# Kernel optimization log

Measured on AMD Instinct MI355X. Metric: run time of the kernel, lower is better.

## Reference

```python
import jax, jax.numpy as jnp
import numpy as np


def _pool_matrix(out_size, in_size):
    # torch AdaptiveAvgPool2d bin edges: start=floor(i*in/out), end=ceil((i+1)*in/out)
    starts = (np.arange(out_size) * in_size) // out_size
    ends = -((-(np.arange(1, out_size + 1) * in_size)) // out_size)
    M = np.zeros((out_size, in_size), np.float32)
    for i in range(out_size):
        M[i, starts[i]:ends[i]] = 1.0 / (ends[i] - starts[i])
    return jnp.asarray(M)


def _cbr(x, w, g, b):
    # 1x1 conv (no bias) + BatchNorm eval (rm=0, rv=1, eps=1e-5) + ReLU6
    y = jnp.einsum('bchw,oc->bohw', x, w)
    y = y * (g / np.sqrt(1.0 + 1e-5))[None, :, None, None] + b[None, :, None, None]
    return jnp.clip(y, 0.0, 6.0)


def _fd_gate(x, g, b, scale):
    # x: [..., L, D]; parameter-free finite-difference gate with residual 0.2
    xp = jnp.pad(x, [(0, 0)] * (x.ndim - 2) + [(1, 0), (0, 0)])[..., :-1, :]
    d = x - xp
    mu = d.mean(-1, keepdims=True)
    var = ((d - mu) ** 2).mean(-1, keepdims=True)
    dn = (d - mu) / jnp.sqrt(var + 1e-5) * g + b
    nd = jnp.sqrt((dn ** 2).sum(-1, keepdims=True)) * scale
    gate = 0.2 + 0.8 * jnp.tanh(jnp.abs(nd))
    return x * gate


def _cross_scan(x):  # [B,C,H,W] -> [B,8,C,H*W]
    B, C, H, W = x.shape
    h = jnp.arange(H)[:, None]
    w = jnp.arange(W)[None, :]
    diag = jnp.broadcast_to(((h + w) % W)[None, None], x.shape)
    anti = jnp.broadcast_to(((w - h) % W)[None, None], x.shape)
    x0 = x.reshape(B, C, H * W)
    x1 = x.transpose(0, 1, 3, 2).reshape(B, C, H * W)
    gd = jnp.take_along_axis(x, diag, -1).transpose(0, 1, 3, 2).reshape(B, C, H * W)
    ga = jnp.take_along_axis(x, anti, -1).transpose(0, 1, 3, 2).reshape(B, C, H * W)
    return jnp.stack([x0, x1, jnp.flip(x0, -1), jnp.flip(x1, -1), gd, ga,
                      jnp.flip(gd, -1), jnp.flip(ga, -1)], 1)


def _cross_merge(ys, gw):  # ys [B,8,D,H,W], gw [B,8] -> [B,D,H*W]
    B, K, D, H, W = ys.shape
    L = H * W
    ys = ys.reshape(B, K, D, L) * gw[:, :, None, None]
    h = jnp.arange(H)[:, None]
    w = jnp.arange(W)[None, :]
    y_h = ys[:, 0] + jnp.flip(ys[:, 2], -1)
    y_v = ys[:, 1] + jnp.flip(ys[:, 3], -1)
    y_v = y_v.reshape(B, D, W, H).transpose(0, 1, 3, 2).reshape(B, D, L)
    y_rb = (y_h + y_v).reshape(B, D, H, W)
    y_d = (ys[:, 4] + jnp.flip(ys[:, 6], -1)).reshape(B, D, W, H).transpose(0, 1, 3, 2)
    y_a = (ys[:, 5] + jnp.flip(ys[:, 7], -1)).reshape(B, D, W, H).transpose(0, 1, 3, 2)
    # scatter along W is the inverse permutation of the diagonal gather
    inv_d = jnp.broadcast_to(((w - h) % W)[None, None], y_d.shape)
    inv_a = jnp.broadcast_to(((w + h) % W)[None, None], y_a.shape)
    s_d = jnp.take_along_axis(y_d, inv_d, -1)
    s_a = jnp.take_along_axis(y_a, inv_a, -1)
    return (y_rb + s_d + s_a).reshape(B, D, L)


def _mamba(params, x):  # x [B,L,Dm] -> [B,L,Dm]
    in_w, cw, cb, xp_w, dtp_w, dtp_b, A_log, Dp, out_w = params
    B, L, Dm = x.shape
    d_inner, d_conv = cw.shape
    d_state = A_log.shape[1]
    dt_rank = dtp_w.shape[1]
    xz = x @ in_w.T                       # [B,L,2*d_inner]
    u, z = jnp.split(xz, 2, axis=-1)
    uc = u.transpose(0, 2, 1)             # [B,d_inner,L]
    up = jnp.pad(uc, ((0, 0), (0, 0), (d_conv - 1, 0)))  # causal depthwise conv
    conv = cb[None, :, None]
    for k in range(d_conv):
        conv = conv + cw[None, :, k, None] * up[:, :, k:k + L]
    u = jax.nn.silu(conv).transpose(0, 2, 1)  # [B,L,d_inner]
    x_dbl = u @ xp_w.T
    dt, Bc, Cc = jnp.split(x_dbl, [dt_rank, dt_rank + d_state], axis=-1)
    dt = jax.nn.softplus(dt @ dtp_w.T + dtp_b)  # [B,L,d_inner]
    A = -jnp.exp(A_log)                         # [d_inner,d_state]

    def step(h, inp):
        dt_t, B_t, C_t, u_t = inp               # [B,d_inner],[B,d_state],[B,d_state],[B,d_inner]
        dA = jnp.exp(dt_t[..., None] * A)
        h = dA * h + (dt_t * u_t)[..., None] * B_t[:, None, :]
        y = jnp.einsum('bds,bs->bd', h, C_t)
        return h, y

    h0 = jnp.zeros((B, d_inner, d_state), x.dtype)
    _, ys = jax.lax.scan(step, h0, (dt.swapaxes(0, 1), Bc.swapaxes(0, 1),
                                    Cc.swapaxes(0, 1), u.swapaxes(0, 1)))
    y = ys.swapaxes(0, 1) + u * Dp
    y = y * jax.nn.silu(z)
    return y @ out_w.T


def setup_inputs() -> dict:
    ks = jax.random.split(jax.random.key(0), 12)
    B, C, H, W = 8, 512, 16, 16
    dim, pool_len = 128, 4
    chs = dim * pool_len + C          # 1024
    d_inner, d_state, d_conv, dt_rank = 2048, 16, 4, 64
    f32 = jnp.float32
    inp = {
        'x': jax.random.normal(ks[0], (B, C, H, W), f32),
        'pw': jax.random.normal(ks[1], (pool_len, dim, C), f32) * 0.05,
        'bn_g': jnp.ones((pool_len, dim), f32),
        'bn_b': jnp.zeros((pool_len, dim), f32),
        'gate_w': jax.random.normal(ks[2], (8, chs), f32) * 0.02,
        'ln_g': jnp.ones((chs,), f32),
        'ln_b': jnp.zeros((chs,), f32),
        'fd_scale': jnp.ones((1,), f32),
        'in_w': jax.random.normal(ks[3], (8, 2 * d_inner, chs), f32) * 0.02,
        'cw': jax.random.normal(ks[4], (8, d_inner, d_conv), f32) * 0.2,
        'cb': jnp.zeros((8, d_inner), f32),
        'xp_w': jax.random.normal(ks[5], (8, dt_rank + 2 * d_state, d_inner), f32) * 0.02,
        'dtp_w': jax.random.normal(ks[6], (8, d_inner, dt_rank), f32) * 0.05,
        'dtp_b': jnp.log(jnp.expm1(jax.random.uniform(ks[7], (8, d_inner), f32, 1e-3, 0.1))),
        'A_log': jnp.broadcast_to(jnp.log(jnp.arange(1, d_state + 1, dtype=f32)), (8, d_inner, d_state)) + 0.0,
        'D_p': jnp.ones((8, d_inner), f32),
        'out_w': jax.random.normal(ks[8], (8, chs, d_inner), f32) * 0.02,
    }
    return inp


def reference(x, pw, bn_g, bn_b, gate_w, ln_g, ln_b, fd_scale,
              in_w, cw, cb, xp_w, dtp_w, dtp_b, A_log, D_p, out_w):
    B, C, H, W = x.shape
    dim = pw.shape[1]
    pools = []
    # pool branch 0: ConvBNReLU then global avg pool then bilinear upsample (constant)
    p0 = _cbr(x, pw[0], bn_g[0], bn_b[0]).mean((2, 3), keepdims=True)
    pools.append(jnp.broadcast_to(p0, (B, dim, H, W)))
    for i, s in enumerate((5, 9, 13)):
        M = _pool_matrix(s, H)
        pooled = jnp.einsum('oh,bchw,pw->bcop', M, x, M)
        y = _cbr(pooled, pw[i + 1], bn_g[i + 1], bn_b[i + 1])
        pools.append(jax.image.resize(y, (B, dim, H, W), 'bilinear'))
    pools.append(x)
    xc = jnp.concatenate(pools, 1)                 # [B, chs, H, W]
    chs = xc.shape[1]
    # MoE gating: softmax over 8 directions, keep top-4
    logits = xc.mean((2, 3)) @ gate_w.T
    scores = jax.nn.softmax(logits, -1)
    vals, idx = jax.lax.top_k(scores, 4)
    gw = jnp.zeros_like(scores).at[jnp.arange(B)[:, None], idx].set(vals)
    xs = _cross_scan(xc).transpose(0, 1, 3, 2)     # [B,8,L,chs]
    xg = _fd_gate(xs, ln_g, ln_b, fd_scale)
    params = (in_w, cw, cb, xp_w, dtp_w, dtp_b, A_log, D_p, out_w)
    ys = jax.vmap(_mamba, in_axes=(0, 1), out_axes=1)(params, xg)  # [B,8,L,chs]
    ys = ys.transpose(0, 1, 3, 2).reshape(B, 8, chs, H, W)
    y = _cross_merge(ys, gw)                       # [B,chs,L]
    return y.reshape(B, chs, H, W)
```

## Files before the change

### kernel.cpp

```cpp
#include <hip/hip_runtime.h>
#include <math.h>

#define DEV __device__ __forceinline__

typedef unsigned short u16;
typedef short bf16x8 __attribute__((ext_vector_type(8)));
typedef float f32x4 __attribute__((ext_vector_type(4)));

DEV float blk_sum(float v, float* sb) {
  #pragma unroll
  for (int o = 32; o > 0; o >>= 1) v += __shfl_down(v, o, 64);
  int lane = threadIdx.x & 63, wid = threadIdx.x >> 6;
  __syncthreads();
  if (lane == 0) sb[wid] = v;
  __syncthreads();
  return sb[0] + sb[1] + sb[2] + sb[3];
}

DEV float silu_f(float x) { return x / (1.f + expf(-x)); }
DEV int imin_i(int a, int b) { return a < b ? a : b; }
DEV int imax_i(int a, int b) { return a > b ? a : b; }

DEV u16 bf_rne(float x) {
  unsigned u = __float_as_uint(x);
  return (u16)((u + 0x7fffu + ((u >> 16) & 1u)) >> 16);
}
DEV float bf_val(u16 h) { return __uint_as_float((unsigned)h << 16); }

DEV void gll16(const void* g, void* l) {
  __builtin_amdgcn_global_load_lds(
      (__attribute__((address_space(1))) void*)(g),
      (__attribute__((address_space(3))) void*)(l), 16, 0, 0);
}

#define BN_SCALE 0.9999950000374997f


__global__ __launch_bounds__(256) void copyx_kernel(const float* __restrict__ x,
                                                    float* __restrict__ xcT) {
  int idx = blockIdx.x * 256 + threadIdx.x;
  int l = idx & 255; int bc = idx >> 8; int c = bc & 511; int b = bc >> 9;
  xcT[((long)b * 256 + l) * 1024 + 512 + c] = x[idx];
}

__global__ __launch_bounds__(256) void pool0_kernel(const float* __restrict__ x,
    const float* __restrict__ pw, const float* __restrict__ bng,
    const float* __restrict__ bnb, float* __restrict__ xcT) {
  __shared__ float sb[8];
  int b = blockIdx.x, o = blockIdx.y, p = threadIdx.x;
  const float* xp = x + (long)b * 512 * 256 + p;
  const float* w = pw + (long)o * 512;
  float s = 0.f;
  for (int c = 0; c < 512; c++) s = fmaf(xp[(long)c * 256], w[c], s);
  float gs = bng[o] * BN_SCALE;
  float v = fminf(fmaxf(fmaf(s, gs, bnb[o]), 0.f), 6.f);
  float m = blk_sum(v, sb) * (1.f / 256.f);
  xcT[((long)b * 256 + p) * 1024 + o] = m;
}

__global__ void apool_kernel(const float* __restrict__ x, float* __restrict__ pooled, int s) {
  int s2 = s * s;
  int idx = blockIdx.x * 256 + threadIdx.x;
  if (idx >= 8 * 512 * s2) return;
  int op = idx % s2; int bc = idx / s2;
  int oh = op / s, ow = op % s;
  int h0 = oh * 16 / s, h1 = (oh * 16 + 16 + s - 1) / s;
  int w0 = ow * 16 / s, w1 = (ow * 16 + 16 + s - 1) / s;
  const float* xp = x + (long)bc * 256;
  float sum = 0.f;
  for (int h = h0; h < h1; h++)
    for (int w = w0; w < w1; w++) sum += xp[h * 16 + w];
  pooled[(long)bc * s2 + op] = sum / (float)((h1 - h0) * (w1 - w0));
}

__global__ void cbr_kernel(const float* __restrict__ pooled, const float* __restrict__ pw_i,
    const float* __restrict__ bng_i, const float* __restrict__ bnb_i,
    float* __restrict__ ys, int s2) {
  int b = blockIdx.x, o = blockIdx.y, p = threadIdx.x;
  if (p >= s2) return;
  const float* pp = pooled + (long)b * 512 * s2 + p;
  const float* w = pw_i + (long)o * 512;
  float sum = 0.f;
  for (int c = 0; c < 512; c++) sum = fmaf(pp[(long)c * s2], w[c], sum);
  float gs = bng_i[o] * BN_SCALE;
  ys[((long)b * 128 + o) * s2 + p] = fminf(fmaxf(fmaf(sum, gs, bnb_i[o]), 0.f), 6.f);
}

__global__ void resize_kernel(const float* __restrict__ ys, float* __restrict__ xcT,
                              int s, int ch0) {
  int b = blockIdx.x, o = blockIdx.y, t = threadIdx.x;
  int h = t >> 4, w = t & 15;
  float scale = (float)s / 16.f;
  float sh = (h + 0.5f) * scale - 0.5f;
  float sw = (w + 0.5f) * scale - 0.5f;
  int h0 = (int)floorf(sh); float fh = sh - (float)h0;
  int w0 = (int)floorf(sw); float fw = sw - (float)w0;
  int ha = imin_i(imax_i(h0, 0), s - 1), hb = imin_i(imax_i(h0 + 1, 0), s - 1);
  int wa = imin_i(imax_i(w0, 0), s - 1), wb = imin_i(imax_i(w0 + 1, 0), s - 1);
  const float* yp = ys + ((long)b * 128 + o) * s * s;
  float v = (1.f - fh) * ((1.f - fw) * yp[ha * s + wa] + fw * yp[ha * s + wb]) +
            fh * ((1.f - fw) * yp[hb * s + wa] + fw * yp[hb * s + wb]);
  xcT[((long)b * 256 + t) * 1024 + ch0 + o] = v;
}

__global__ __launch_bounds__(256) void xcmean_kernel(const float* __restrict__ xcT,
                                                     float* __restrict__ xm) {
  int idx = blockIdx.x * 256 + threadIdx.x;
  int c = idx & 1023; int b = idx >> 10;
  const float* p = xcT + (long)b * 256 * 1024 + c;
  float s = 0.f;
  for (int l = 0; l < 256; l++) s += p[(long)l * 1024];
  xm[idx] = s * (1.f / 256.f);
}

__global__ void gate_kernel(const float* __restrict__ xm, const float* __restrict__ gww,
                            float* __restrict__ gwout) {
  __shared__ float lg[64];
  int t = threadIdx.x;
  int b = t >> 3, j = t & 7;
  const float* xb = xm + b * 1024;
  const float* wj = gww + j * 1024;
  float s = 0.f;
  for (int c = 0; c < 1024; c++) s = fmaf(xb[c], wj[c], s);
  lg[t] = s;
  __syncthreads();
  if (t < 8) {
    float v[8], mx = -1e30f;
    for (int i = 0; i < 8; i++) { v[i] = lg[t * 8 + i]; mx = fmaxf(mx, v[i]); }
    float den = 0.f;
    for (int i = 0; i < 8; i++) { v[i] = expf(v[i] - mx); den += v[i]; }
    float inv = 1.f / den;
    float out[8], tmp[8];
    for (int i = 0; i < 8; i++) { out[i] = 0.f; tmp[i] = v[i] * inv; }
    for (int it = 0; it < 4; it++) {
      int bi = 0; float bv = tmp[0];
      for (int i = 1; i < 8; i++) if (tmp[i] > bv) { bv = tmp[i]; bi = i; }
      out[bi] = bv; tmp[bi] = -1e30f;
    }
    for (int i = 0; i < 8; i++) gwout[t * 8 + i] = out[i];
  }
}


DEV int scan_src(int k, int l) {
  switch (k) {
    case 0: return l;
    case 1: return ((l & 15) << 4) | (l >> 4);
    case 2: return 255 - l;
    case 3: { int l2 = 255 - l; return ((l2 & 15) << 4) | (l2 >> 4); }
    case 4: { int h = l & 15, w = l >> 4; return (h << 4) | ((h + w) & 15); }
    case 5: { int h = l & 15, w = l >> 4; return (h << 4) | ((w - h) & 15); }
    case 6: { int l2 = 255 - l; int h = l2 & 15, w = l2 >> 4; return (h << 4) | ((h + w) & 15); }
    default:{ int l2 = 255 - l; int h = l2 & 15, w = l2 >> 4; return (h << 4) | ((w - h) & 15); }
  }
}

__global__ __launch_bounds__(256) void fd_gate_kernel(const float* __restrict__ xcT,
    const float* __restrict__ lng, const float* __restrict__ lnb,
    const float* __restrict__ fsc, u16* __restrict__ xghi, u16* __restrict__ xglo,
    int k0, const float* __restrict__ gw) {
  __shared__ float sb[8];
  int l = blockIdx.x;
  int rg = blockIdx.y;
  int kk = rg >> 3, b = rg & 7;
  int k = k0 + kk;
  if (gw[b * 8 + k] == 0.f) return;
  int t = threadIdx.x;
  int p = scan_src(k, l);
  float4 cv = *((const float4*)(xcT + ((long)b * 256 + p) * 1024) + t);
  float4 pv = make_float4(0.f, 0.f, 0.f, 0.f);
  if (l > 0) {
    int pm = scan_src(k, l - 1);
    pv = *((const float4*)(xcT + ((long)b * 256 + pm) * 1024) + t);
  }
  float d0 = cv.x - pv.x, d1 = cv.y - pv.y, d2 = cv.z - pv.z, d3 = cv.w - pv.w;
  float mu = blk_sum(d0 + d1 + d2 + d3, sb) * (1.f / 1024.f);
  float e0 = d0 - mu, e1 = d1 - mu, e2 = d2 - mu, e3 = d3 - mu;
  float var = blk_sum(e0*e0 + e1*e1 + e2*e2 + e3*e3, sb) * (1.f / 1024.f);
  float rstd = rsqrtf(var + 1e-5f);
  float4 g4 = *((const float4*)lng + t);
  float4 b4 = *((const float4*)lnb + t);
  float n0 = fmaf(e0 * rstd, g4.x, b4.x);
  float n1 = fmaf(e1 * rstd, g4.y, b4.y);
  float n2 = fmaf(e2 * rstd, g4.z, b4.z);
  float n3 = fmaf(e3 * rstd, g4.w, b4.w);
  float ss = blk_sum(n0*n0 + n1*n1 + n2*n2 + n3*n3, sb);
  float nd = sqrtf(ss) * fsc[0];
  float gate = 0.2f + 0.8f * tanhf(fabsf(nd));
  float o0 = cv.x * gate, o1 = cv.y * gate, o2 = cv.z * gate, o3 = cv.w * gate;
  ushort4 h4, l4;
  h4.x = bf_rne(o0); l4.x = bf_rne(o0 - bf_val(h4.x));
  h4.y = bf_rne(o1); l4.y = bf_rne(o1 - bf_val(h4.y));
  h4.z = bf_rne(o2); l4.z = bf_rne(o2 - bf_val(h4.z));
  h4.w = bf_rne(o3); l4.w = bf_rne(o3 - bf_val(h4.w));
  long off = ((long)rg * 256 + l) * 1024;
  ((ushort4*)(xghi + off))[t] = h4;
  ((ushort4*)(xglo + off))[t] = l4;
}

__global__ __launch_bounds__(256) void split_kernel(const float* __restrict__ src,
    u16* __restrict__ hi, u16* __restrict__ lo, long n4) {
  long i = (long)blockIdx.x * 256 + threadIdx.x;
  if (i >= n4) return;
  float4 v = ((const float4*)src)[i];
  ushort4 h, l;
  h.x = bf_rne(v.x); l.x = bf_rne(v.x - bf_val(h.x));
  h.y = bf_rne(v.y); l.y = bf_rne(v.y - bf_val(h.y));
  h.z = bf_rne(v.z); l.z = bf_rne(v.z - bf_val(h.z));
  h.w = bf_rne(v.w); l.w = bf_rne(v.w - bf_val(h.w));
  ((ushort4*)hi)[i] = h;
  ((ushort4*)lo)[i] = l;
}

template<int EPI>
__global__ __launch_bounds__(256) void gemm_x3(
    const u16* __restrict__ Ahi, const u16* __restrict__ Alo, long aS,
    const u16* __restrict__ Bhi, const u16* __restrict__ Blo, long bS,
    float* __restrict__ C, long cS, int K, int ldc,
    int k0, const float* __restrict__ gw) {
  const long m_blk = (long)blockIdx.x * 128;
  const int z = blockIdx.z;
  {
    int b = (int)(m_blk >> 8);
    int k = k0 + z;
    if (gw[b * 8 + k] == 0.f) return;
  }
  __shared__ u16 As[2][4096];
  __shared__ u16 Bs[2][4096];
  const int t = threadIdx.x;
  Ahi += (long)z * aS; Alo += (long)z * aS;
  Bhi += (long)z * bS; Blo += (long)z * bS; C += (long)z * cS;
  const long n_blk = (long)blockIdx.y * 128;
  const int lane = t & 63, wid = t >> 6;
  const int wm = (wid >> 1) * 64, wn = (wid & 1) * 64;
  const int srow = t >> 2, sseg = (t & 3) * 8;
  const u16* gAh = Ahi + (m_blk + srow) * (long)K + sseg;
  const u16* gAl = Alo + (m_blk + srow) * (long)K + sseg;
  const u16* gBh = Bhi + (n_blk + srow) * (long)K + sseg;
  const u16* gBl = Blo + (n_blk + srow) * (long)K + sseg;
  const int lb = wid * 512;
  const long k64 = (long)64 * K;
  f32x4 acc[4][4];
  #pragma unroll
  for (int r = 0; r < 4; r++)
    #pragma unroll
    for (int c = 0; c < 4; c++) acc[r][c] = (f32x4)0.f;
  const int a_m = lane & 15, a_k = (lane >> 4) * 8;

  for (int kt = 0; kt < K; kt += 32) {
    __syncthreads();
    gll16(gAh + kt,        &As[0][lb]);
    gll16(gAh + kt + k64,  &As[0][lb + 2048]);
    gll16(gAl + kt,        &As[1][lb]);
    gll16(gAl + kt + k64,  &As[1][lb + 2048]);
    gll16(gBh + kt,        &Bs[0][lb]);
    gll16(gBh + kt + k64,  &Bs[0][lb + 2048]);
    gll16(gBl + kt,        &Bs[1][lb]);
    gll16(gBl + kt + k64,  &Bs[1][lb + 2048]);
    __syncthreads();
    bf16x8 ah[4], al[4], bh[4], bl[4];
    #pragma unroll
    for (int r = 0; r < 4; r++) {
      int row = wm + r * 16 + a_m;
      ah[r] = *(const bf16x8*)&As[0][row * 32 + a_k];
      al[r] = *(const bf16x8*)&As[1][row * 32 + a_k];
    }
    #pragma unroll
    for (int c = 0; c < 4; c++) {
      int row = wn + c * 16 + a_m;
      bh[c] = *(const bf16x8*)&Bs[0][row * 32 + a_k];
      bl[c] = *(const bf16x8*)&Bs[1][row * 32 + a_k];
    }
    #pragma unroll
    for (int r = 0; r < 4; r++)
      #pragma unroll
      for (int c = 0; c < 4; c++) {
        acc[r][c] = __builtin_amdgcn_mfma_f32_16x16x32_bf16(ah[r], bh[c], acc[r][c], 0, 0, 0);
        acc[r][c] = __builtin_amdgcn_mfma_f32_16x16x32_bf16(ah[r], bl[c], acc[r][c], 0, 0, 0);
        acc[r][c] = __builtin_amdgcn_mfma_f32_16x16x32_bf16(al[r], bh[c], acc[r][c], 0, 0, 0);
      }
  }
  const bool dosilu = (EPI == 1) && (n_blk >= 2048);
  const int c_col = lane & 15, c_row = (lane >> 4) * 4;
  #pragma unroll
  for (int r = 0; r < 4; r++) {
    long row0 = m_blk + wm + r * 16 + c_row;
    #pragma unroll
    for (int c = 0; c < 4; c++) {
      long col = n_blk + wn + c * 16 + c_col;
      float* cp = C + row0 * ldc + col;
      #pragma unroll
      for (int q = 0; q < 4; q++) {
        float v = acc[r][c][q];
        if (dosilu) v = silu_f(v);
        cp[(long)q * ldc] = v;
      }
    }
  }
}

template<int EPI>
__global__ __launch_bounds__(256) void gemm_nt(
    const float* __restrict__ A, long lda, long aK,
    const float* __restrict__ Bw, long bK,
    float* __restrict__ C, long ldc, long cK,
    int N, int Kd,
    const float* __restrict__ bias, long biasK,
    int k0, const float* __restrict__ gw) {
  const int m_blk = blockIdx.x * 128;
  const int kk = blockIdx.z;
  {
    int b = m_blk >> 8;
    if (gw[b * 8 + k0 + kk] == 0.f) return;
  }
  __shared__ float As2[16][132];
  __shared__ float Bs2[16][68];
  const int t = threadIdx.x;
  A += (long)kk * aK; Bw += (long)kk * bK; C += (long)kk * cK;
  if (EPI == 1) bias += (long)kk * biasK;
  const int n_blk = blockIdx.y * 64;
  const int tx = t & 15, ty = t >> 4;
  const int aq = t & 3, ar = t >> 2;
  float acc[8][4];
  #pragma unroll
  for (int i = 0; i < 8; i++)
    #pragma unroll
    for (int j = 0; j < 4; j++) acc[i][j] = 0.f;

  for (int kt = 0; kt < Kd; kt += 16) {
    float4 a0 = *(const float4*)(A + (long)(m_blk + ar) * lda + kt + aq * 4);
    float4 a1 = *(const float4*)(A + (long)(m_blk + 64 + ar) * lda + kt + aq * 4);
    float4 b0 = make_float4(0.f, 0.f, 0.f, 0.f);
    int bn = n_blk + ar;
    if (bn < N) b0 = *(const float4*)(Bw + (long)bn * Kd + kt + aq * 4);
    __syncthreads();
    As2[aq*4+0][ar] = a0.x; As2[aq*4+1][ar] = a0.y; As2[aq*4+2][ar] = a0.z; As2[aq*4+3][ar] = a0.w;
    As2[aq*4+0][64+ar] = a1.x; As2[aq*4+1][64+ar] = a1.y; As2[aq*4+2][64+ar] = a1.z; As2[aq*4+3][64+ar] = a1.w;
    Bs2[aq*4+0][ar] = b0.x; Bs2[aq*4+1][ar] = b0.y; Bs2[aq*4+2][ar] = b0.z; Bs2[aq*4+3][ar] = b0.w;
    __syncthreads();
    #pragma unroll
    for (int k2 = 0; k2 < 16; k2++) {
      float av[8], bv[4];
      #pragma unroll
      for (int i = 0; i < 8; i++) av[i] = As2[k2][ty * 8 + i];
      #pragma unroll
      for (int j = 0; j < 4; j++) bv[j] = Bs2[k2][tx * 4 + j];
      #pragma unroll
      for (int i = 0; i < 8; i++)
        #pragma unroll
        for (int j = 0; j < 4; j++) acc[i][j] = fmaf(av[i], bv[j], acc[i][j]);
    }
  }
  #pragma unroll
  for (int i = 0; i < 8; i++) {
    long m = m_blk + ty * 8 + i;
    #pragma unroll
    for (int j = 0; j < 4; j++) {
      int n = n_blk + tx * 4 + j;
      if (n < N) {
        float v = acc[i][j];
        if (EPI == 1) {
          v += bias[n];
          v = log1pf(expf(-fabsf(v))) + fmaxf(v, 0.f);
        }
        C[m * ldc + n] = v;
      }
    }
  }
}

__global__ __launch_bounds__(256) void conv_silu_kernel(float* uz,
    const float* __restrict__ cw, const float* __restrict__ cb, int k0,
    const float* __restrict__ gw) {
  long tid = (long)blockIdx.x * 256 + threadIdx.x;
  int d = (int)(tid & 2047);
  long rg = tid >> 11;
  int k = k0 + (int)(rg >> 3);
  int b = (int)(rg & 7);
  if (gw[b * 8 + k] == 0.f) return;
  const float* w = cw + ((long)k * 2048 + d) * 4;
  float w0 = w[0], w1 = w[1], w2 = w[2], w3 = w[3];
  float bias = cb[(long)k * 2048 + d];
  float* base = uz + rg * 256 * 4096 + d;
  float x0 = 0.f, x1 = 0.f, x2 = 0.f;
  #pragma unroll 4
  for (int l = 0; l < 256; l++) {
    float x3 = base[(long)l * 4096];
    float v = bias + w0 * x0 + w1 * x1 + w2 * x2 + w3 * x3;
    base[(long)l * 4096] = silu_f(v);
    x0 = x1; x1 = x2; x2 = x3;
  }
}

__global__ __launch_bounds__(256) void scan_kernel(
    const float* __restrict__ dt, const float* __restrict__ uz,
    const float* __restrict__ xdbl, const float* __restrict__ A_log,
    const float* __restrict__ Dp, u16* __restrict__ yhi, u16* __restrict__ ylo,
    int k0, const float* __restrict__ gw) {
  int rg = blockIdx.y;
  int k = k0 + (rg >> 3);
  int b = rg & 7;
  if (gw[b * 8 + k] == 0.f) return;
  int t = threadIdx.x;
  int d = blockIdx.x * 256 + t;
  float Av[16];
  const float* Ap = A_log + ((long)k * 2048 + d) * 16;
  #pragma unroll
  for (int s = 0; s < 16; s++) Av[s] = -expf(Ap[s]);
  float dp = Dp[(long)k * 2048 + d];
  __shared__ float BC[8][32];
  float h[16];
  #pragma unroll
  for (int s = 0; s < 16; s++) h[s] = 0.f;
  long rbase = (long)rg * 256;
  for (int l8 = 0; l8 < 256; l8 += 8) {
    __syncthreads();
    BC[t >> 5][t & 31] = xdbl[(rbase + l8 + (t >> 5)) * 96 + 64 + (t & 31)];
    __syncthreads();
    #pragma unroll
    for (int j = 0; j < 8; j++) {
      long r = rbase + l8 + j;
      float dtv = dt[r * 2048 + d];
      float uv = uz[r * 4096 + d];
      float zs = uz[r * 4096 + 2048 + d];
      float dtu = dtv * uv;
      float y = 0.f;
      #pragma unroll
      for (int s = 0; s < 16; s++) {
        float dA = expf(dtv * Av[s]);
        h[s] = fmaf(dA, h[s], dtu * BC[j][s]);
        y = fmaf(h[s], BC[j][16 + s], y);
      }
      float ov = (y + uv * dp) * zs;
      u16 hv = bf_rne(ov);
      yhi[r * 2048 + d] = hv;
      ylo[r * 2048 + d] = bf_rne(ov - bf_val(hv));
    }
  }
}

__global__ __launch_bounds__(256) void merge_kernel(const float* __restrict__ yo,
    const float* __restrict__ gw, float* __restrict__ out, int k0, int NK) {
  int b = blockIdx.x; int c0 = blockIdx.y * 4; int t = threadIdx.x;
  int h = t >> 4, w = t & 15;
  int l0 = t;
  int l1 = (w << 4) | h;
  int l4 = (((w - h) & 15) << 4) | h;
  int l5 = (((w + h) & 15) << 4) | h;
  int lk[8] = { l0, l1, 255 - l0, 255 - l1, l4, l5, 255 - l4, 255 - l5 };
  float a0 = 0.f, a1 = 0.f, a2 = 0.f, a3 = 0.f;
  for (int kk = 0; kk < NK; kk++) {
    int k = k0 + kk;
    float g = gw[b * 8 + k];
    if (g == 0.f) continue;
    const float4 p = *(const float4*)(yo + (((long)kk * 8 + b) * 256 + lk[k]) * 1024 + c0);
    a0 = fmaf(g, p.x, a0); a1 = fmaf(g, p.y, a1); a2 = fmaf(g, p.z, a2); a3 = fmaf(g, p.w, a3);
  }
  float* op = out + ((long)b * 1024 + c0) * 256 + t;
  if (k0 == 0) { op[0] = a0; op[256] = a1; op[512] = a2; op[768] = a3; }
  else         { op[0] += a0; op[256] += a1; op[512] += a2; op[768] += a3; }
}

extern "C" void kernel_launch(void* const* d_in, const int* in_sizes, int n_in,
                              void* d_out, int out_size, void* d_ws, size_t ws_size,
                              hipStream_t stream) {
  (void)in_sizes; (void)n_in; (void)out_size;
  const float* x      = (const float*)d_in[0];
  const float* pw     = (const float*)d_in[1];
  const float* bn_g   = (const float*)d_in[2];
  const float* bn_b   = (const float*)d_in[3];
  const float* gate_w = (const float*)d_in[4];
  const float* ln_g   = (const float*)d_in[5];
  const float* ln_b   = (const float*)d_in[6];
  const float* fd_s   = (const float*)d_in[7];
  const float* in_w   = (const float*)d_in[8];
  const float* cw     = (const float*)d_in[9];
  const float* cb     = (const float*)d_in[10];
  const float* xp_w   = (const float*)d_in[11];
  const float* dtp_w  = (const float*)d_in[12];
  const float* dtp_b  = (const float*)d_in[13];
  const float* A_log  = (const float*)d_in[14];
  const float* D_p    = (const float*)d_in[15];
  const float* out_w  = (const float*)d_in[16];
  float* out = (float*)d_out;
  float* ws = (float*)d_ws;

  size_t off = 0;
  auto alloc = [&](size_t n) { float* p = ws + off; off += n; return p; };
  float* xcT    = alloc(2097152);
  float* pooled = alloc((size_t)8 * 512 * 169);
  float* ysb    = alloc((size_t)8 * 128 * 169);
  float* xm     = alloc(8192);
  float* gwb    = alloc(64);
  const size_t fixed = off;

  const size_t PK_XGP  = 1048576;
  const size_t PK_UZ   = 8388608;
  const size_t PK_DT   = 4194304;
  const size_t PK_YP   = 2097152;
  const size_t PK_XD   = 196608;
  const size_t PK_YO   = 2097152;
  const size_t PK_INWP = 2097152;
  const size_t PK_OUWP = 1048576;
  const size_t perk = 2*PK_XGP + PK_UZ + PK_DT + 2*PK_YP + PK_XD + PK_YO
                    + 2*PK_INWP + 2*PK_OUWP;
  const size_t avail = ws_size / sizeof(float);
  int NK = 8;
  while (NK > 1 && fixed + perk * (size_t)NK > avail) NK >>= 1;

  u16* xghi  = (u16*)alloc(PK_XGP * NK);
  u16* xglo  = (u16*)alloc(PK_XGP * NK);
  float* uzb = alloc(PK_UZ * NK);
  float* dtb = alloc(PK_DT * NK);
  u16* yhi   = (u16*)alloc(PK_YP * NK);
  u16* ylo   = (u16*)alloc(PK_YP * NK);
  float* xdb = alloc(PK_XD * NK);
  float* yob = alloc(PK_YO * NK);
  u16* inwhi = (u16*)alloc(PK_INWP * NK);
  u16* inwlo = (u16*)alloc(PK_INWP * NK);
  u16* ouwhi = (u16*)alloc(PK_OUWP * NK);
  u16* ouwlo = (u16*)alloc(PK_OUWP * NK);

  copyx_kernel<<<4096, 256, 0, stream>>>(x, xcT);
  pool0_kernel<<<dim3(8, 128), 256, 0, stream>>>(x, pw, bn_g, bn_b, xcT);
  const int svals[3] = {5, 9, 13};
  for (int i = 0; i < 3; i++) {
    int s = svals[i], s2 = s * s;
    int tot = 8 * 512 * s2;
    apool_kernel<<<(tot + 255) / 256, 256, 0, stream>>>(x, pooled, s);
    cbr_kernel<<<dim3(8, 128), 256, 0, stream>>>(pooled, pw + (long)(i + 1) * 128 * 512,
                                                 bn_g + (i + 1) * 128, bn_b + (i + 1) * 128,
                                                 ysb, s2);
    resize_kernel<<<dim3(8, 128), 256, 0, stream>>>(ysb, xcT, s, 128 * (i + 1));
  }
  xcmean_kernel<<<32, 256, 0, stream>>>(xcT, xm);
  gate_kernel<<<1, 64, 0, stream>>>(xm, gate_w, gwb);

  for (int k0 = 0; k0 < 8; k0 += NK) {
    {
      long n4 = (long)NK * 4096 * 1024 / 4;
      split_kernel<<<(int)((n4 + 255) / 256), 256, 0, stream>>>(
          in_w + (long)k0 * 4096 * 1024, inwhi, inwlo, n4);
      long m4 = (long)NK * 1024 * 2048 / 4;
      split_kernel<<<(int)((m4 + 255) / 256), 256, 0, stream>>>(
          out_w + (long)k0 * 1024 * 2048, ouwhi, ouwlo, m4);
    }
    fd_gate_kernel<<<dim3(256, NK * 8), 256, 0, stream>>>(xcT, ln_g, ln_b, fd_s,
                                                          xghi, xglo, k0, gwb);
    gemm_x3<1><<<dim3(16, 32, NK), 256, 0, stream>>>(
        xghi, xglo, (long)2 * PK_XGP,
        inwhi, inwlo, (long)2 * PK_INWP,
        uzb, (long)PK_UZ, 1024, 4096, k0, gwb);
    conv_silu_kernel<<<NK * 64, 256, 0, stream>>>(uzb, cw, cb, k0, gwb);
    gemm_nt<0><<<dim3(16, 2, NK), 256, 0, stream>>>(
        uzb, 4096, (long)PK_UZ, xp_w + (long)k0 * 96 * 2048, (long)96 * 2048,
        xdb, 96, (long)PK_XD, 96, 2048, nullptr, 0, k0, gwb);
    gemm_nt<1><<<dim3(16, 1, NK), 256, 0, stream>>>(
        xdb, 96, (long)PK_XD, dtp_w + (long)k0 * 2048 * 64, (long)2048 * 64,
        dtb, 2048, (long)PK_DT, 2048, 64, dtp_b + (long)k0 * 2048, 2048, k0, gwb);
    scan_kernel<<<dim3(8, NK * 8), 256, 0, stream>>>(dtb, uzb, xdb, A_log, D_p,
                                                     yhi, ylo, k0, gwb);
    gemm_x3<0><<<dim3(16, 8, NK), 256, 0, stream>>>(
        yhi, ylo, (long)2 * PK_YP,
        ouwhi, ouwlo, (long)2 * PK_OUWP,
        yob, (long)PK_YO, 2048, 1024, k0, gwb);
    merge_kernel<<<dim3(8, 256), 256, 0, stream>>>(yob, gwb, out, k0, NK);
  }
}
```

Before: 1.980 ms.

## Split scan state across lanes, MFMA x_proj GEMM, chunked conv emitting bf16 pairs

The selective scan now spreads the 16 state entries of each channel over 4 lane groups and sums the partial outputs with shuffles. This quadruples the block count and cuts per-thread register use. The depthwise conv is cut into 32-row chunks for more parallelism, and it writes the activated input as a bf16 hi/lo pair instead of updating fp32 in place. The x_proj matmul then runs on the 3-pass bf16 MFMA GEMM, using a padded, pre-split copy of its weights, instead of the fp32 SIMT GEMM. The trade-offs are an extra weight-split launch, padded work on the N dimension, and rounding the scan input to a bf16 hi/lo pair.

```diff
diff --git a/kernel.cpp b/kernel.cpp
--- a/kernel.cpp
+++ b/kernel.cpp
@@ -212,11 +212,33 @@
   ((ushort4*)lo)[i] = l;
 }
 
+__global__ __launch_bounds__(256) void xpw_split_kernel(const float* __restrict__ xpw,
+    u16* __restrict__ hi, u16* __restrict__ lo, int k0, int NK) {
+  long idx = (long)blockIdx.x * 256 + threadIdx.x;
+  long per = 128 * 2048 / 4;
+  long tot = (long)NK * per;
+  if (idx >= tot) return;
+  long kk = idx / per;
+  long rem = idx - kk * per;
+  long row = rem / 512;
+  long col4 = rem - row * 512;
+  float4 v = make_float4(0.f, 0.f, 0.f, 0.f);
+  if (row < 96)
+    v = *(const float4*)(xpw + (((long)(k0 + kk) * 96 + row) * 2048) + col4 * 4);
+  ushort4 h, l;
+  h.x = bf_rne(v.x); l.x = bf_rne(v.x - bf_val(h.x));
+  h.y = bf_rne(v.y); l.y = bf_rne(v.y - bf_val(h.y));
+  h.z = bf_rne(v.z); l.z = bf_rne(v.z - bf_val(h.z));
+  h.w = bf_rne(v.w); l.w = bf_rne(v.w - bf_val(h.w));
+  ((ushort4*)hi)[idx] = h;
+  ((ushort4*)lo)[idx] = l;
+}
+
 template<int EPI>
 __global__ __launch_bounds__(256) void gemm_x3(
     const u16* __restrict__ Ahi, const u16* __restrict__ Alo, long aS,
     const u16* __restrict__ Bhi, const u16* __restrict__ Blo, long bS,
-    float* __restrict__ C, long cS, int K, int ldc,
+    float* __restrict__ C, long cS, int K, int ldc, int Nlim,
     int k0, const float* __restrict__ gw) {
   const long m_blk = (long)blockIdx.x * 128;
   const int z = blockIdx.z;
@@ -288,6 +310,7 @@
     #pragma unroll
     for (int c = 0; c < 4; c++) {
       long col = n_blk + wn + c * 16 + c_col;
+      if (col >= Nlim) continue;
       float* cp = C + row0 * ldc + col;
       #pragma unroll
       for (int q = 0; q < 4; q++) {
@@ -369,25 +392,36 @@
   }
 }
 
-__global__ __launch_bounds__(256) void conv_silu_kernel(float* uz,
-    const float* __restrict__ cw, const float* __restrict__ cb, int k0,
+__global__ __launch_bounds__(256) void conv_split_kernel(const float* __restrict__ uz,
+    const float* __restrict__ cw, const float* __restrict__ cb,
+    u16* __restrict__ uhi, u16* __restrict__ ulo, int k0,
     const float* __restrict__ gw) {
   long tid = (long)blockIdx.x * 256 + threadIdx.x;
   int d = (int)(tid & 2047);
-  long rg = tid >> 11;
-  int k = k0 + (int)(rg >> 3);
-  int b = (int)(rg & 7);
+  int chunk = (int)((tid >> 11) & 7);
+  int rg = (int)(tid >> 14);
+  int k = k0 + (rg >> 3);
+  int b = rg & 7;
   if (gw[b * 8 + k] == 0.f) return;
   const float* w = cw + ((long)k * 2048 + d) * 4;
   float w0 = w[0], w1 = w[1], w2 = w[2], w3 = w[3];
   float bias = cb[(long)k * 2048 + d];
-  float* base = uz + rg * 256 * 4096 + d;
+  long r0 = (long)rg * 256 + chunk * 32;
   float x0 = 0.f, x1 = 0.f, x2 = 0.f;
+  if (chunk > 0) {
+    x0 = uz[(r0 - 3) * 4096 + d];
+    x1 = uz[(r0 - 2) * 4096 + d];
+    x2 = uz[(r0 - 1) * 4096 + d];
+  }
   #pragma unroll 4
-  for (int l = 0; l < 256; l++) {
-    float x3 = base[(long)l * 4096];
+  for (int l = 0; l < 32; l++) {
+    long r = r0 + l;
+    float x3 = uz[r * 4096 + d];
     float v = bias + w0 * x0 + w1 * x1 + w2 * x2 + w3 * x3;
-    base[(long)l * 4096] = silu_f(v);
+    float sv = silu_f(v);
+    u16 hv = bf_rne(sv);
+    uhi[r * 2048 + d] = hv;
+    ulo[r * 2048 + d] = bf_rne(sv - bf_val(hv));
     x0 = x1; x1 = x2; x2 = x3;
   }
 }
@@ -402,16 +436,16 @@
   int b = rg & 7;
   if (gw[b * 8 + k] == 0.f) return;
   int t = threadIdx.x;
-  int d = blockIdx.x * 256 + t;
-  float Av[16];
-  const float* Ap = A_log + ((long)k * 2048 + d) * 16;
+  int lane = t & 63, wid = t >> 6;
+  int sg = lane >> 4, dl = lane & 15;
+  int d = blockIdx.x * 64 + wid * 16 + dl;
+  float Av[4];
+  const float* Ap = A_log + ((long)k * 2048 + d) * 16 + sg * 4;
   #pragma unroll
-  for (int s = 0; s < 16; s++) Av[s] = -expf(Ap[s]);
+  for (int s = 0; s < 4; s++) Av[s] = -expf(Ap[s]);
   float dp = Dp[(long)k * 2048 + d];
   __shared__ float BC[8][32];
-  float h[16];
-  #pragma unroll
-  for (int s = 0; s < 16; s++) h[s] = 0.f;
+  float h[4] = {0.f, 0.f, 0.f, 0.f};
   long rbase = (long)rg * 256;
   for (int l8 = 0; l8 < 256; l8 += 8) {
     __syncthreads();
@@ -421,20 +455,24 @@
     for (int j = 0; j < 8; j++) {
       long r = rbase + l8 + j;
       float dtv = dt[r * 2048 + d];
-      float uv = uz[r * 4096 + d];
+      float uv = bf_val(yhi[r * 2048 + d]) + bf_val(ylo[r * 2048 + d]);
       float zs = uz[r * 4096 + 2048 + d];
       float dtu = dtv * uv;
       float y = 0.f;
       #pragma unroll
-      for (int s = 0; s < 16; s++) {
+      for (int s = 0; s < 4; s++) {
         float dA = expf(dtv * Av[s]);
-        h[s] = fmaf(dA, h[s], dtu * BC[j][s]);
-        y = fmaf(h[s], BC[j][16 + s], y);
+        h[s] = fmaf(dA, h[s], dtu * BC[j][sg * 4 + s]);
+        y = fmaf(h[s], BC[j][16 + sg * 4 + s], y);
       }
-      float ov = (y + uv * dp) * zs;
-      u16 hv = bf_rne(ov);
-      yhi[r * 2048 + d] = hv;
-      ylo[r * 2048 + d] = bf_rne(ov - bf_val(hv));
+      y += __shfl_xor(y, 16, 64);
+      y += __shfl_xor(y, 32, 64);
+      if (sg == 0) {
+        float ov = (y + uv * dp) * zs;
+        u16 hv = bf_rne(ov);
+        yhi[r * 2048 + d] = hv;
+        ylo[r * 2048 + d] = bf_rne(ov - bf_val(hv));
+      }
     }
   }
 }
@@ -502,8 +540,9 @@
   const size_t PK_YO   = 2097152;
   const size_t PK_INWP = 2097152;
   const size_t PK_OUWP = 1048576;
+  const size_t PK_XPWP = 131072;
   const size_t perk = 2*PK_XGP + PK_UZ + PK_DT + 2*PK_YP + PK_XD + PK_YO
-                    + 2*PK_INWP + 2*PK_OUWP;
+                    + 2*PK_INWP + 2*PK_OUWP + 2*PK_XPWP;
   const size_t avail = ws_size / sizeof(float);
   int NK = 8;
   while (NK > 1 && fixed + perk * (size_t)NK > avail) NK >>= 1;
@@ -520,6 +559,8 @@
   u16* inwlo = (u16*)alloc(PK_INWP * NK);
   u16* ouwhi = (u16*)alloc(PK_OUWP * NK);
   u16* ouwlo = (u16*)alloc(PK_OUWP * NK);
+  u16* xpwhi = (u16*)alloc(PK_XPWP * NK);
+  u16* xpwlo = (u16*)alloc(PK_XPWP * NK);
 
   copyx_kernel<<<4096, 256, 0, stream>>>(x, xcT);
   pool0_kernel<<<dim3(8, 128), 256, 0, stream>>>(x, pw, bn_g, bn_b, xcT);
@@ -544,26 +585,30 @@
       long m4 = (long)NK * 1024 * 2048 / 4;
       split_kernel<<<(int)((m4 + 255) / 256), 256, 0, stream>>>(
           out_w + (long)k0 * 1024 * 2048, ouwhi, ouwlo, m4);
+      long p4 = (long)NK * 128 * 2048 / 4;
+      xpw_split_kernel<<<(int)((p4 + 255) / 256), 256, 0, stream>>>(
+          xp_w, xpwhi, xpwlo, k0, NK);
     }
     fd_gate_kernel<<<dim3(256, NK * 8), 256, 0, stream>>>(xcT, ln_g, ln_b, fd_s,
                                                           xghi, xglo, k0, gwb);
     gemm_x3<1><<<dim3(16, 32, NK), 256, 0, stream>>>(
         xghi, xglo, (long)2 * PK_XGP,
         inwhi, inwlo, (long)2 * PK_INWP,
-        uzb, (long)PK_UZ, 1024, 4096, k0, gwb);
-    conv_silu_kernel<<<NK * 64, 256, 0, stream>>>(uzb, cw, cb, k0, gwb);
-    gemm_nt<0><<<dim3(16, 2, NK), 256, 0, stream>>>(
-        uzb, 4096, (long)PK_UZ, xp_w + (long)k0 * 96 * 2048, (long)96 * 2048,
-        xdb, 96, (long)PK_XD, 96, 2048, nullptr, 0, k0, gwb);
+        uzb, (long)PK_UZ, 1024, 4096, 4096, k0, gwb);
+    conv_split_kernel<<<NK * 512, 256, 0, stream>>>(uzb, cw, cb, yhi, ylo, k0, gwb);
+    gemm_x3<0><<<dim3(16, 1, NK), 256, 0, stream>>>(
+        yhi, ylo, (long)2 * PK_YP,
+        xpwhi, xpwlo, (long)2 * PK_XPWP,
+        xdb, (long)PK_XD, 2048, 96, 96, k0, gwb);
     gemm_nt<1><<<dim3(16, 1, NK), 256, 0, stream>>>(
         xdb, 96, (long)PK_XD, dtp_w + (long)k0 * 2048 * 64, (long)2048 * 64,
         dtb, 2048, (long)PK_DT, 2048, 64, dtp_b + (long)k0 * 2048, 2048, k0, gwb);
-    scan_kernel<<<dim3(8, NK * 8), 256, 0, stream>>>(dtb, uzb, xdb, A_log, D_p,
-                                                     yhi, ylo, k0, gwb);
+    scan_kernel<<<dim3(32, NK * 8), 256, 0, stream>>>(dtb, uzb, xdb, A_log, D_p,
+                                                      yhi, ylo, k0, gwb);
     gemm_x3<0><<<dim3(16, 8, NK), 256, 0, stream>>>(
         yhi, ylo, (long)2 * PK_YP,
         ouwhi, ouwlo, (long)2 * PK_OUWP,
-        yob, (long)PK_YO, 2048, 1024, k0, gwb);
+        yob, (long)PK_YO, 2048, 1024, 1024, k0, gwb);
     merge_kernel<<<dim3(8, 256), 256, 0, stream>>>(yob, gwb, out, k0, NK);
   }
 }
```

After: 1.850 ms. -6.6%, faster.
